# Optimization experiments

Hardware: AMD Instinct MI355X
Metric: run time of the kernel (lower is better)

The kernel has to match this reference:

```python
import jax, jax.numpy as jnp
import numpy as np
import math

B, S, E, H = 2, 2048, 1024, 16
D = E // H  # d_head = 64

def setup_inputs() -> dict:
    key = jax.random.key(0)
    ks = jax.random.split(key, 7)
    query = jax.random.normal(ks[0], (B, S, E), dtype=jnp.float32)
    k_in = jax.random.normal(ks[1], (B, S, E), dtype=jnp.float32)
    v_in = jax.random.normal(ks[2], (B, S, E), dtype=jnp.float32)
    # causal mask, broadcastable over batch and heads; mask==0 positions are blocked
    mask = jnp.tril(jnp.ones((S, S), dtype=jnp.int32))[None, None]
    scale = 1.0 / math.sqrt(E)
    w_q = jax.random.normal(ks[3], (E, E), dtype=jnp.float32) * scale
    w_k = jax.random.normal(ks[4], (E, E), dtype=jnp.float32) * scale
    w_v = jax.random.normal(ks[5], (E, E), dtype=jnp.float32) * scale
    w_o = jax.random.normal(ks[6], (E, E), dtype=jnp.float32) * scale
    return {"query": query, "key": k_in, "value": v_in, "mask": mask,
            "w_q": w_q, "w_k": w_k, "w_v": w_v, "w_o": w_o}

def reference(query, key, value, mask, w_q, w_k, w_v, w_o):
    # projections (nn.Linear with no bias: x @ W^T); split heads -> [B,H,S,D]
    q = (query @ w_q.T).reshape(B, S, H, D).transpose(0, 2, 1, 3)
    k = (key @ w_k.T).reshape(B, S, H, D).transpose(0, 2, 1, 3)
    v = (value @ w_v.T).reshape(B, S, H, D).transpose(0, 2, 1, 3)
    # scaled dot-product scores [B,H,S,S]
    scores = jnp.einsum('bhqd,bhkd->bhqk', q, k) / math.sqrt(D)
    scores = jnp.where(mask == 0, jnp.float32(-1e9), scores)
    attn = jax.nn.softmax(scores, axis=-1)  # dropout p=0.0 -> identity
    out = jnp.einsum('bhqk,bhkd->bhqd', attn, v)  # [B,H,S,D]
    out = out.transpose(0, 2, 1, 3).reshape(B, S, E)
    return out @ w_o.T
```

## Files before the change

kernel.cpp:

```cpp
#include <hip/hip_runtime.h>
#include <hip/hip_bf16.h>

#define B_ 2
#define S_ 2048
#define E_ 1024
#define H_ 16
#define D_ 64

typedef __attribute__((ext_vector_type(8))) short bf16x8;
typedef __attribute__((ext_vector_type(4))) float f32x4;

static __device__ __forceinline__ unsigned short f2bf(float x) {
    union { float f; unsigned u; } v; v.f = x;
    unsigned r = v.u + 0x7FFF + ((v.u >> 16) & 1);
    return (unsigned short)(r >> 16);
}

static __device__ __forceinline__ unsigned pack2bf(float a, float b) {
    union { float f; unsigned u; } x, y; x.f = a; y.f = b;
    unsigned ra = x.u + 0x7FFF + ((x.u >> 16) & 1);
    unsigned rb = y.u + 0x7FFF + ((y.u >> 16) & 1);
    return (ra >> 16) | (rb & 0xFFFF0000u);
}

static __device__ __forceinline__ unsigned packtrunc(float a, float b) {
    union { float f; unsigned u; } x, y; x.f = a; y.f = b;
    return __builtin_amdgcn_perm(y.u, x.u, 0x07060302);
}

static __device__ __forceinline__ void async_copy16(const void* gsrc, void* ldst) {
    __builtin_amdgcn_global_load_lds(
        (const __attribute__((address_space(1))) void*)gsrc,
        (__attribute__((address_space(3))) void*)ldst, 16, 0, 0);
}

__global__ void cvt_all(const float* __restrict__ s0, const float* __restrict__ s1,
                        const float* __restrict__ s2, const float* __restrict__ s3,
                        const float* __restrict__ s4, const float* __restrict__ s5,
                        const float* __restrict__ s6,
                        unsigned short* __restrict__ xdst, unsigned short* __restrict__ wdst,
                        float scq) {
    int b = blockIdx.x;
    const float* src; unsigned short* dst; int i; float c = 1.f;
    if (b < 12288) {
        int ti = b >> 12, lb = b & 4095;
        src = (ti == 0) ? s0 : (ti == 1) ? s1 : s2;
        dst = xdst + (size_t)ti * 4194304;
        i = lb * 256 + threadIdx.x;
    } else {
        int r = b - 12288, ti = r >> 10, lb = r & 1023;
        src = (ti == 0) ? s3 : (ti == 1) ? s4 : (ti == 2) ? s5 : s6;
        dst = wdst + (size_t)ti * 1048576;
        i = lb * 256 + threadIdx.x;
        if (ti == 0) c = scq;
    }
    float4 f = ((const float4*)src)[i];
    ushort4 o;
    o.x = f2bf(f.x * c); o.y = f2bf(f.y * c); o.z = f2bf(f.z * c); o.w = f2bf(f.w * c);
    ((ushort4*)dst)[i] = o;
}

__global__ __launch_bounds__(512, 2) void gemm256(
    const unsigned short* __restrict__ A0, const unsigned short* __restrict__ B0,
    void* __restrict__ C0) {
    __shared__ __align__(16) unsigned short L[65536];
    const int z = blockIdx.z;
    const unsigned short* A  = A0 + (size_t)z * 4194304;
    const unsigned short* Bm = B0 + (size_t)z * 1048576;
    const int o = (int)(blockIdx.x + (blockIdx.y << 2));
    const int cx = o & 7, tx = o >> 3;
    const int bm = (cx * 2 + (tx >> 2)) * 256;
    const int bn = (tx & 3) * 256;
    const int tid = threadIdx.x;
    const int w = tid >> 6, lane = tid & 63;
    const int wr = w >> 2, wc = w & 3;
    const int col = lane & 15, quad = lane >> 4;
    const int r0 = tid >> 3, cg = (tid & 7) ^ (r0 & 7);
    const size_t aR = (size_t)(bm + r0) * 1024 + cg * 8;
    const size_t bR = (size_t)(bn + r0) * 1024 + cg * 8;
    const int l0 = tid * 8, l1 = tid * 8 + 4096;
    const int ach = (quad ^ (col & 7)) * 8;
    const int aRd = wr * 8192 + col * 64 + ach;
    const int bRd = 32768 + (wc >> 1) * 8192 + (wc & 1) * 4096 + col * 64 + ach;

    f32x4 acc[8][4] = {};
    bf16x8 bA[4][2], bB0[2][2], bB1[2][2];

#define STAGE_A(d, h, t) do { \
    async_copy16(A + aR + (size_t)((h) * 128) * 1024 + (t) * 64, &L[((d) * 2 + (h)) * 8192 + l0]); \
    async_copy16(A + aR + (size_t)((h) * 128 + 64) * 1024 + (t) * 64, &L[((d) * 2 + (h)) * 8192 + l1]); \
} while (0)
#define STAGE_B(d, h, t) do { \
    async_copy16(Bm + bR + (size_t)((h) * 128) * 1024 + (t) * 64, &L[32768 + ((d) * 2 + (h)) * 8192 + l0]); \
    async_copy16(Bm + bR + (size_t)((h) * 128 + 64) * 1024 + (t) * 64, &L[32768 + ((d) * 2 + (h)) * 8192 + l1]); \
} while (0)
#define RD_A(d, mh) do { _Pragma("unroll") for (int i = 0; i < 4; i++) { \
    bA[i][0] = *(const bf16x8*)&L[(d) * 16384 + (mh) * 4096 + i * 1024 + aRd]; \
    bA[i][1] = *(const bf16x8*)&L[(d) * 16384 + (mh) * 4096 + i * 1024 + (aRd ^ 32)]; } } while (0)
#define RD_B(d, nh, BB) do { _Pragma("unroll") for (int j = 0; j < 2; j++) { \
    BB[j][0] = *(const bf16x8*)&L[(d) * 16384 + (nh) * 2048 + j * 1024 + bRd]; \
    BB[j][1] = *(const bf16x8*)&L[(d) * 16384 + (nh) * 2048 + j * 1024 + (bRd ^ 32)]; } } while (0)
#define MM(m0, BB, n0) do { __builtin_amdgcn_s_setprio(1); \
    _Pragma("unroll") for (int i = 0; i < 4; i++) _Pragma("unroll") for (int j = 0; j < 2; j++) { \
        acc[(m0) + i][(n0) + j] = __builtin_amdgcn_mfma_f32_16x16x32_bf16(bA[i][0], BB[j][0], acc[(m0) + i][(n0) + j], 0, 0, 0); \
        acc[(m0) + i][(n0) + j] = __builtin_amdgcn_mfma_f32_16x16x32_bf16(bA[i][1], BB[j][1], acc[(m0) + i][(n0) + j], 0, 0, 0); } \
    __builtin_amdgcn_s_setprio(0); } while (0)
#define BARX __builtin_amdgcn_s_barrier()
#define VMW asm volatile("s_waitcnt vmcnt(4)" ::: "memory")

    STAGE_B(0, 0, 0); STAGE_B(0, 1, 0);
    STAGE_A(0, 0, 0); STAGE_A(0, 1, 0);
    STAGE_B(1, 0, 1); STAGE_B(1, 1, 1);
    VMW; BARX;

#pragma unroll 1
    for (int j = 0; j < 8; j++) {
        const int to = 2 * j + 1;
        const int tn = (2 * j + 2 < 16) ? 2 * j + 2 : 15;
        const int tm = (2 * j + 3 < 16) ? 2 * j + 3 : 15;
        STAGE_A(1, 0, to); RD_A(0, 0); RD_B(0, 0, bB0); BARX; MM(0, bB0, 0); BARX;
        STAGE_A(1, 1, to); RD_B(0, 1, bB1);             BARX; MM(0, bB1, 2); BARX;
        STAGE_B(0, 0, tn); RD_A(0, 1);                  BARX; MM(4, bB1, 2); BARX;
        STAGE_B(0, 1, tn);                              BARX; MM(4, bB0, 0); VMW; BARX;
        STAGE_A(0, 0, tn); RD_A(1, 0); RD_B(1, 0, bB0); BARX; MM(0, bB0, 0); BARX;
        STAGE_A(0, 1, tn); RD_B(1, 1, bB1);             BARX; MM(0, bB1, 2); BARX;
        STAGE_B(1, 0, tm); RD_A(1, 1);                  BARX; MM(4, bB1, 2); BARX;
        STAGE_B(1, 1, tm);                              BARX; MM(4, bB0, 0); VMW; BARX;
    }
#undef STAGE_A
#undef STAGE_B
#undef RD_A
#undef RD_B
#undef MM
#undef BARX
#undef VMW

    __syncthreads();

    unsigned short* scr = &L[w * 8192];
    const int grow0 = bm + wr * 128;
    const int b  = grow0 >> 11;
    const int s0 = grow0 & 2047;
    const int hh = (bn + wc * 64) >> 6;
    unsigned short* outp = (unsigned short*)C0 + (size_t)z * 4194304;
    if (z == 2) {
#pragma unroll
        for (int mi = 0; mi < 8; mi++)
#pragma unroll
            for (int nj = 0; nj < 4; nj++) {
                int n = nj * 16 + col;
                int c = mi * 2 + (quad >> 1);
                uint2 pk;
                pk.x = pack2bf(acc[mi][nj][0], acc[mi][nj][1]);
                pk.y = pack2bf(acc[mi][nj][2], acc[mi][nj][3]);
                *(uint2*)&scr[n * 128 + ((c ^ (n & 7)) << 3) + ((quad & 1) << 2)] = pk;
            }
        asm volatile("s_waitcnt lgkmcnt(0)" ::: "memory");
#pragma unroll
        for (int it = 0; it < 16; it++) {
            int slot = it * 64 + lane, n = slot >> 4, c = slot & 15;
            uint4 v = *(uint4*)&scr[n * 128 + ((c ^ (n & 7)) << 3)];
            *(uint4*)&outp[(((size_t)b * H_ + hh) * D_ + n) * S_ + s0 + c * 8] = v;
        }
    } else {
#pragma unroll
        for (int mi = 0; mi < 8; mi++)
#pragma unroll
            for (int nj = 0; nj < 4; nj++)
#pragma unroll
                for (int r = 0; r < 4; r++) {
                    int m = mi * 16 + quad * 4 + r, n = nj * 16 + col;
                    scr[m * 64 + (((n >> 3) ^ (m & 7)) << 3) + (n & 7)] = f2bf(acc[mi][nj][r]);
                }
        asm volatile("s_waitcnt lgkmcnt(0)" ::: "memory");
#pragma unroll
        for (int it = 0; it < 16; it++) {
            int slot = it * 64 + lane, m = slot >> 3, c = slot & 7;
            uint4 v = *(uint4*)&scr[m * 64 + ((c ^ (m & 7)) << 3)];
            *(uint4*)&outp[(((size_t)b * H_ + hh) * S_ + s0 + m) * (size_t)D_ + c * 8] = v;
        }
    }
}

template <int MODE>
__global__ __launch_bounds__(256) void gemm128(
    const unsigned short* __restrict__ A0, const unsigned short* __restrict__ B0,
    void* __restrict__ C0, int M, int N, int K) {
    __shared__ __align__(16) unsigned short KV[8][4096];
    const unsigned short* A = A0;
    const unsigned short* Bm = B0;
    const int o = (int)(blockIdx.x + (blockIdx.y << 3));
    const int cx = o & 7, tx = o >> 3;
    const int bm = ((cx << 2) + (tx >> 3)) * 128;
    const int bn = (tx & 7) * 128;
    const int tid = threadIdx.x;
    const int w = tid >> 6, lane = tid & 63;
    const int col = lane & 15, quad = lane >> 4;
    const int wm = (w >> 1) * 64, wn = (w & 1) * 64;
    const int cq = (quad ^ ((col >> 1) & 3)) << 3;

    f32x4 acc[4][4] = {};

    const int r0 = tid >> 2;
    const int cg = (tid & 3) ^ ((r0 >> 1) & 3);
    const size_t aoff0 = (size_t)(bm + r0) * K + cg * 8;
    const size_t aoff1 = (size_t)(bm + r0 + 64) * K + cg * 8;
    const size_t boff0 = (size_t)(bn + r0) * K + cg * 8;
    const size_t boff1 = (size_t)(bn + r0 + 64) * K + cg * 8;
    const int l0 = tid * 8, l1 = (tid + 256) * 8;

    const int nk = K >> 5;

    async_copy16(A  + aoff0,      &KV[0][l0]);
    async_copy16(A  + aoff1,      &KV[0][l1]);
    async_copy16(Bm + boff0,      &KV[4][l0]);
    async_copy16(Bm + boff1,      &KV[4][l1]);
    async_copy16(A  + aoff0 + 32, &KV[1][l0]);
    async_copy16(A  + aoff1 + 32, &KV[1][l1]);
    async_copy16(Bm + boff0 + 32, &KV[5][l0]);
    async_copy16(Bm + boff1 + 32, &KV[5][l1]);

    for (int kt = 0; kt < nk; kt++) {
        {
            const int kp = kt + 2;
            const int src = (kp < nk) ? kp : (nk - 1);
            const int bp = kp & 3;
            const size_t ko = (size_t)src * 32;
            async_copy16(A  + aoff0 + ko, &KV[bp][l0]);
            async_copy16(A  + aoff1 + ko, &KV[bp][l1]);
            async_copy16(Bm + boff0 + ko, &KV[4 + bp][l0]);
            async_copy16(Bm + boff1 + ko, &KV[4 + bp][l1]);
        }
        asm volatile("s_waitcnt vmcnt(8)" ::: "memory");
        __builtin_amdgcn_s_barrier();

        const unsigned short* Ab = &KV[kt & 3][0];
        const unsigned short* Bb = &KV[4 + (kt & 3)][0];
        bf16x8 af[4], bfr[4];
#pragma unroll
        for (int i = 0; i < 4; i++) af[i]  = *(const bf16x8*)&Ab[(wm + i * 16 + col) * 32 + cq];
#pragma unroll
        for (int j = 0; j < 4; j++) bfr[j] = *(const bf16x8*)&Bb[(wn + j * 16 + col) * 32 + cq];
#pragma unroll
        for (int i = 0; i < 4; i++)
#pragma unroll
            for (int j = 0; j < 4; j++)
                acc[i][j] = __builtin_amdgcn_mfma_f32_16x16x32_bf16(af[i], bfr[j], acc[i][j], 0, 0, 0);
    }

    __syncthreads();

    if (MODE == 3) {
#pragma unroll
        for (int i = 0; i < 4; i++)
#pragma unroll
            for (int j = 0; j < 4; j++)
#pragma unroll
                for (int r = 0; r < 4; r++) {
                    int gm = bm + wm + i * 16 + quad * 4 + r;
                    int gn = bn + wn + j * 16 + col;
                    ((float*)C0)[(size_t)gm * N + gn] = acc[i][j][r];
                }
    }
}

__global__ __launch_bounds__(512) void attn_kernel(
    const unsigned short* __restrict__ Q, const unsigned short* __restrict__ K_,
    const unsigned short* __restrict__ Vt, unsigned short* __restrict__ Out) {
    __shared__ __align__(16) unsigned short KV[8][4096];
    __shared__ __align__(16) float Lred[4][2][64];
    const int o = (int)(blockIdx.x + (blockIdx.y << 4));
    const int cx = o & 7, tx = o >> 3;
    const int hloc = (tx >> 1) & 3;
    const int f_ = (tx ^ (tx >> 5)) & 1;
    const int G_ = (((tx >> 4) & 1) << 2) | (((tx >> 3) & 1) << 1) | (tx & 1);
    const int qb = f_ ? (G_ ^ 15) : G_;
    const int bh = (cx << 2) + hloc;
    const int q0 = qb * 128;
    const int tid = threadIdx.x;
    const int w = tid >> 6, lane = tid & 63;
    const int qg = w >> 1, kh = w & 1, kh32 = kh << 5;
    const int col = lane & 15, quad = lane >> 4, swz = col & 7;
    const int qw0 = q0 + qg * 32;
    const float NINF = -__builtin_huge_valf();

    const unsigned short* Qh = Q + (size_t)bh * S_ * D_;
    const unsigned short* Kh = K_ + (size_t)bh * S_ * D_;
    const unsigned short* Vh = Vt + (size_t)bh * D_ * S_;

    bf16x8 qf[2][2];
#pragma unroll
    for (int i = 0; i < 2; i++)
#pragma unroll
        for (int h = 0; h < 2; h++)
            qf[i][h] = *(const bf16x8*)(Qh + (size_t)(qw0 + i * 16 + col) * 64 + h * 32 + quad * 8);

    f32x4 o_[2][4] = {};
    float lsum[2] = {0.f, 0.f};

    const int sRow = tid >> 3, sCg = (tid & 7) ^ (sRow & 7);
    const size_t koff = (size_t)sRow * 64 + sCg * 8;
    const size_t voff = (size_t)sRow * S_ + sCg * 8;
    const int ldsoff = tid * 8;

    const int nk = 2 * (qb + 1);

    async_copy16(Kh + koff, &KV[0][ldsoff]);
    async_copy16(Vh + voff, &KV[4][ldsoff]);
    async_copy16(Kh + koff + 64 * 64, &KV[1][ldsoff]);
    async_copy16(Vh + voff + 64, &KV[5][ldsoff]);

    for (int kt = 0; kt < nk; kt++) {
        const int k0 = kt * 64;
        {
            const int kp = kt + 2;
            const int src = (kp < nk) ? kp : (nk - 1);
            const int bp = kp & 3;
            async_copy16(Kh + koff + (size_t)src * 4096, &KV[bp][ldsoff]);
            async_copy16(Vh + voff + (size_t)src * 64, &KV[4 + bp][ldsoff]);
        }
        asm volatile("s_waitcnt vmcnt(4)" ::: "memory");
        __builtin_amdgcn_s_barrier();

        if (k0 + kh32 > qw0 + 31) continue;

        const unsigned short* Kb = &KV[kt & 3][0];
        const unsigned short* Vb = &KV[4 + (kt & 3)][0];

        f32x4 sc[2][2] = {};
        __builtin_amdgcn_s_setprio(1);
#pragma unroll
        for (int h = 0; h < 2; h++) {
            const int cq = ((h * 4 + quad) ^ swz) * 8;
#pragma unroll
            for (int ct = 0; ct < 2; ct++) {
                bf16x8 kf = *(const bf16x8*)&Kb[(kh32 + ct * 16 + col) * 64 + cq];
                sc[0][ct] = __builtin_amdgcn_mfma_f32_16x16x32_bf16(kf, qf[0][h], sc[0][ct], 0, 0, 0);
                sc[1][ct] = __builtin_amdgcn_mfma_f32_16x16x32_bf16(kf, qf[1][h], sc[1][ct], 0, 0, 0);
            }
        }
        __builtin_amdgcn_s_setprio(0);
        if (k0 + kh32 + 31 <= qw0) {
#pragma unroll
            for (int i = 0; i < 2; i++)
#pragma unroll
                for (int ct = 0; ct < 2; ct++) {
#pragma unroll
                    for (int r = 0; r < 4; r++)
                        sc[i][ct][r] = __builtin_amdgcn_exp2f(sc[i][ct][r]);
                    lsum[i] += (sc[i][ct][0] + sc[i][ct][1]) + (sc[i][ct][2] + sc[i][ct][3]);
                }
        } else {
#pragma unroll
            for (int i = 0; i < 2; i++)
#pragma unroll
                for (int ct = 0; ct < 2; ct++) {
#pragma unroll
                    for (int r = 0; r < 4; r++) {
                        int key = k0 + kh32 + ct * 16 + quad * 4 + r;
                        int qidx = qw0 + i * 16 + col;
                        float s = (key <= qidx) ? sc[i][ct][r] : NINF;
                        sc[i][ct][r] = __builtin_amdgcn_exp2f(s);
                    }
                    lsum[i] += (sc[i][ct][0] + sc[i][ct][1]) + (sc[i][ct][2] + sc[i][ct][3]);
                }
        }
        union { bf16x8 v; unsigned u[4]; } pf[2];
#pragma unroll
        for (int i = 0; i < 2; i++) {
            pf[i].u[0] = packtrunc(sc[i][0][0], sc[i][0][1]);
            pf[i].u[1] = packtrunc(sc[i][0][2], sc[i][0][3]);
            pf[i].u[2] = packtrunc(sc[i][1][0], sc[i][1][1]);
            pf[i].u[3] = packtrunc(sc[i][1][2], sc[i][1][3]);
        }
        __builtin_amdgcn_s_setprio(1);
#pragma unroll
        for (int dt = 0; dt < 4; dt++) {
            const int row = dt * 16 + col;
            const int ko0 = kh32 + quad * 4;
            const int ko1 = ko0 + 16;
            union { bf16x8 v; uint2 d2[2]; } vf;
            vf.d2[0] = *(const uint2*)&Vb[row * 64 + (((ko0 >> 3) ^ (row & 7)) << 3) + (ko0 & 7)];
            vf.d2[1] = *(const uint2*)&Vb[row * 64 + (((ko1 >> 3) ^ (row & 7)) << 3) + (ko1 & 7)];
#pragma unroll
            for (int i = 0; i < 2; i++)
                o_[i][dt] = __builtin_amdgcn_mfma_f32_16x16x32_bf16(vf.v, pf[i].v, o_[i][dt], 0, 0, 0);
        }
        __builtin_amdgcn_s_setprio(0);
    }

    __syncthreads();
    if (kh == 1) {
        f32x4* R = (f32x4*)&KV[0][0] + qg * 512 + lane * 8;
#pragma unroll
        for (int i = 0; i < 2; i++)
#pragma unroll
            for (int dt = 0; dt < 4; dt++) R[i * 4 + dt] = o_[i][dt];
        Lred[qg][0][lane] = lsum[0];
        Lred[qg][1][lane] = lsum[1];
    }
    __syncthreads();
    if (kh == 0) {
        f32x4* R = (f32x4*)&KV[0][0] + qg * 512 + lane * 8;
#pragma unroll
        for (int i = 0; i < 2; i++)
#pragma unroll
            for (int dt = 0; dt < 4; dt++) o_[i][dt] += R[i * 4 + dt];
        lsum[0] += Lred[qg][0][lane];
        lsum[1] += Lred[qg][1][lane];

        const int b = bh >> 4, hh = bh & 15;
#pragma unroll
        for (int i = 0; i < 2; i++) {
            float l = lsum[i];
            l += __shfl_xor(l, 16);
            l += __shfl_xor(l, 32);
            float inv = 1.f / l;
            int gq = qw0 + i * 16 + col;
#pragma unroll
            for (int dt = 0; dt < 4; dt++) {
                uint2 pk;
                pk.x = pack2bf(o_[i][dt][0] * inv, o_[i][dt][1] * inv);
                pk.y = pack2bf(o_[i][dt][2] * inv, o_[i][dt][3] * inv);
                *(uint2*)&Out[((size_t)b * S_ + gq) * E_ + hh * 64 + dt * 16 + quad * 4] = pk;
            }
        }
    }
}

extern "C" void kernel_launch(void* const* d_in, const int* in_sizes, int n_in,
                              void* d_out, int out_size, void* d_ws, size_t ws_size,
                              hipStream_t stream) {
    const float* query = (const float*)d_in[0];
    const float* key_i = (const float*)d_in[1];
    const float* value = (const float*)d_in[2];
    const float* w_q = (const float*)d_in[4];
    const float* w_k = (const float*)d_in[5];
    const float* w_v = (const float*)d_in[6];
    const float* w_o = (const float*)d_in[7];
    float* out = (float*)d_out;

    const int M = B_ * S_;
    const int N = E_, K = E_;

    char* ws = (char*)d_ws;
    unsigned short* xq  = (unsigned short*)(ws);
    unsigned short* wqb = (unsigned short*)(ws + (24u << 20));
    unsigned short* Qb  = (unsigned short*)(ws + (32u << 20));
    unsigned short* Kb  = (unsigned short*)(ws + (40u << 20));
    unsigned short* Vtb = (unsigned short*)(ws + (48u << 20));
    unsigned short* Ab  = (unsigned short*)(ws + (56u << 20));

    const float SCQ = 0.125f * 1.44269504088896f;

    cvt_all<<<16384, 256, 0, stream>>>(query, key_i, value, w_q, w_k, w_v, w_o,
                                       xq, wqb, SCQ);

    gemm256<<<dim3(4, 16, 3), 512, 0, stream>>>(xq, wqb, Qb);

    attn_kernel<<<dim3(S_ / 128, B_ * H_), 512, 0, stream>>>(Qb, Kb, Vtb, Ab);

    gemm128<3><<<dim3(8, 32), 256, 0, stream>>>(
        Ab, wqb + 3u * 1048576u, out, M, N, K);
}
```

Measured before the change: 204.6 us.

## Software-pipeline attention loop: overlap QK^T of tile t with softmax/PV of t-1

Restructures the attention inner loop so each iteration computes the QK^T scores for the current key tile while running exp, pack and PV MFMAs for the previous tile, using two ping-pong score register sets and a manually unrolled-by-two loop. V tiles are now prefetched one step ahead instead of two, and V is stored so one 16-byte LDS read replaces two 8-byte reads. It also sets a waves-per-EU hint in launch_bounds and changes the transposed V store in the projection epilogue to permute key positions to match the new V fragment layout. The aim is to hide MFMA and exp latency behind each other, at the cost of higher register pressure and a more fragile buffer-reuse schedule.

Result: no change. 202.5 us (-1.0%).

```diff
diff --git a/kernel.cpp b/kernel.cpp
--- a/kernel.cpp
+++ b/kernel.cpp
@@ -157,10 +157,14 @@
             }
         asm volatile("s_waitcnt lgkmcnt(0)" ::: "memory");
 #pragma unroll
-        for (int it = 0; it < 16; it++) {
-            int slot = it * 64 + lane, n = slot >> 4, c = slot & 15;
-            uint4 v = *(uint4*)&scr[n * 128 + ((c ^ (n & 7)) << 3)];
-            *(uint4*)&outp[(((size_t)b * H_ + hh) * D_ + n) * S_ + s0 + c * 8] = v;
+        for (int it = 0; it < 32; it++) {
+            int slot = it * 64 + lane;
+            int n = slot >> 5, u = slot & 31;
+            int grp = u >> 3, T = u & 7;
+            int kpos = grp * 32 + (T & 1) * 16 + ((T >> 1) & 3) * 4;
+            int c = kpos >> 3, off = kpos & 7;
+            uint2 v = *(uint2*)&scr[n * 128 + ((c ^ (n & 7)) << 3) + off];
+            *(uint2*)&outp[(((size_t)b * H_ + hh) * D_ + n) * S_ + s0 + grp * 32 + T * 4] = v;
         }
     } else {
 #pragma unroll
@@ -264,7 +268,7 @@
     }
 }
 
-__global__ __launch_bounds__(512) void attn_kernel(
+__global__ __launch_bounds__(512, 4) void attn_kernel(
     const unsigned short* __restrict__ Q, const unsigned short* __restrict__ K_,
     const unsigned short* __restrict__ Vt, unsigned short* __restrict__ Out) {
     __shared__ __align__(16) unsigned short KV[8][4096];
@@ -297,97 +301,90 @@
 
     f32x4 o_[2][4] = {};
     float lsum[2] = {0.f, 0.f};
+    f32x4 scA[2][2], scB[2][2];
 
     const int sRow = tid >> 3, sCg = (tid & 7) ^ (sRow & 7);
     const size_t koff = (size_t)sRow * 64 + sCg * 8;
     const size_t voff = (size_t)sRow * S_ + sCg * 8;
     const int ldsoff = tid * 8;
+    const int vch = ((kh * 4 + quad) ^ (col & 7)) << 3;
 
     const int nk = 2 * (qb + 1);
 
     async_copy16(Kh + koff, &KV[0][ldsoff]);
+    async_copy16(Kh + koff + 4096, &KV[1][ldsoff]);
     async_copy16(Vh + voff, &KV[4][ldsoff]);
-    async_copy16(Kh + koff + 64 * 64, &KV[1][ldsoff]);
-    async_copy16(Vh + voff + 64, &KV[5][ldsoff]);
-
-    for (int kt = 0; kt < nk; kt++) {
-        const int k0 = kt * 64;
-        {
-            const int kp = kt + 2;
-            const int src = (kp < nk) ? kp : (nk - 1);
-            const int bp = kp & 3;
-            async_copy16(Kh + koff + (size_t)src * 4096, &KV[bp][ldsoff]);
-            async_copy16(Vh + voff + (size_t)src * 64, &KV[4 + bp][ldsoff]);
-        }
-        asm volatile("s_waitcnt vmcnt(4)" ::: "memory");
-        __builtin_amdgcn_s_barrier();
-
-        if (k0 + kh32 > qw0 + 31) continue;
-
-        const unsigned short* Kb = &KV[kt & 3][0];
-        const unsigned short* Vb = &KV[4 + (kt & 3)][0];
-
-        f32x4 sc[2][2] = {};
-        __builtin_amdgcn_s_setprio(1);
-#pragma unroll
-        for (int h = 0; h < 2; h++) {
-            const int cq = ((h * 4 + quad) ^ swz) * 8;
-#pragma unroll
-            for (int ct = 0; ct < 2; ct++) {
-                bf16x8 kf = *(const bf16x8*)&Kb[(kh32 + ct * 16 + col) * 64 + cq];
-                sc[0][ct] = __builtin_amdgcn_mfma_f32_16x16x32_bf16(kf, qf[0][h], sc[0][ct], 0, 0, 0);
-                sc[1][ct] = __builtin_amdgcn_mfma_f32_16x16x32_bf16(kf, qf[1][h], sc[1][ct], 0, 0, 0);
-            }
-        }
-        __builtin_amdgcn_s_setprio(0);
-        if (k0 + kh32 + 31 <= qw0) {
-#pragma unroll
-            for (int i = 0; i < 2; i++)
-#pragma unroll
-                for (int ct = 0; ct < 2; ct++) {
-#pragma unroll
-                    for (int r = 0; r < 4; r++)
-                        sc[i][ct][r] = __builtin_amdgcn_exp2f(sc[i][ct][r]);
-                    lsum[i] += (sc[i][ct][0] + sc[i][ct][1]) + (sc[i][ct][2] + sc[i][ct][3]);
-                }
-        } else {
-#pragma unroll
-            for (int i = 0; i < 2; i++)
-#pragma unroll
-                for (int ct = 0; ct < 2; ct++) {
-#pragma unroll
-                    for (int r = 0; r < 4; r++) {
-                        int key = k0 + kh32 + ct * 16 + quad * 4 + r;
-                        int qidx = qw0 + i * 16 + col;
-                        float s = (key <= qidx) ? sc[i][ct][r] : NINF;
-                        sc[i][ct][r] = __builtin_amdgcn_exp2f(s);
-                    }
-                    lsum[i] += (sc[i][ct][0] + sc[i][ct][1]) + (sc[i][ct][2] + sc[i][ct][3]);
-                }
-        }
-        union { bf16x8 v; unsigned u[4]; } pf[2];
-#pragma unroll
-        for (int i = 0; i < 2; i++) {
-            pf[i].u[0] = packtrunc(sc[i][0][0], sc[i][0][1]);
-            pf[i].u[1] = packtrunc(sc[i][0][2], sc[i][0][3]);
-            pf[i].u[2] = packtrunc(sc[i][1][0], sc[i][1][1]);
-            pf[i].u[3] = packtrunc(sc[i][1][2], sc[i][1][3]);
-        }
-        __builtin_amdgcn_s_setprio(1);
-#pragma unroll
-        for (int dt = 0; dt < 4; dt++) {
-            const int row = dt * 16 + col;
-            const int ko0 = kh32 + quad * 4;
-            const int ko1 = ko0 + 16;
-            union { bf16x8 v; uint2 d2[2]; } vf;
-            vf.d2[0] = *(const uint2*)&Vb[row * 64 + (((ko0 >> 3) ^ (row & 7)) << 3) + (ko0 & 7)];
-            vf.d2[1] = *(const uint2*)&Vb[row * 64 + (((ko1 >> 3) ^ (row & 7)) << 3) + (ko1 & 7)];
-#pragma unroll
-            for (int i = 0; i < 2; i++)
-                o_[i][dt] = __builtin_amdgcn_mfma_f32_16x16x32_bf16(vf.v, pf[i].v, o_[i][dt], 0, 0, 0);
-        }
-        __builtin_amdgcn_s_setprio(0);
-    }
+
+#define APROC(T, PRV) do { \
+    const int k0p = (T) * 64; \
+    if (k0p + kh32 + 31 <= qw0) { \
+        _Pragma("unroll") for (int i2 = 0; i2 < 2; i2++) \
+        _Pragma("unroll") for (int c2 = 0; c2 < 2; c2++) { \
+            _Pragma("unroll") for (int r2 = 0; r2 < 4; r2++) \
+                PRV[i2][c2][r2] = __builtin_amdgcn_exp2f(PRV[i2][c2][r2]); \
+            lsum[i2] += (PRV[i2][c2][0] + PRV[i2][c2][1]) + (PRV[i2][c2][2] + PRV[i2][c2][3]); } \
+    } else { \
+        _Pragma("unroll") for (int i2 = 0; i2 < 2; i2++) \
+        _Pragma("unroll") for (int c2 = 0; c2 < 2; c2++) { \
+            _Pragma("unroll") for (int r2 = 0; r2 < 4; r2++) { \
+                int key = k0p + kh32 + c2 * 16 + quad * 4 + r2; \
+                int qidx = qw0 + i2 * 16 + col; \
+                float sv = (key <= qidx) ? PRV[i2][c2][r2] : NINF; \
+                PRV[i2][c2][r2] = __builtin_amdgcn_exp2f(sv); } \
+            lsum[i2] += (PRV[i2][c2][0] + PRV[i2][c2][1]) + (PRV[i2][c2][2] + PRV[i2][c2][3]); } \
+    } \
+    union { bf16x8 v; unsigned u[4]; } pf[2]; \
+    _Pragma("unroll") for (int i2 = 0; i2 < 2; i2++) { \
+        pf[i2].u[0] = packtrunc(PRV[i2][0][0], PRV[i2][0][1]); \
+        pf[i2].u[1] = packtrunc(PRV[i2][0][2], PRV[i2][0][3]); \
+        pf[i2].u[2] = packtrunc(PRV[i2][1][0], PRV[i2][1][1]); \
+        pf[i2].u[3] = packtrunc(PRV[i2][1][2], PRV[i2][1][3]); } \
+    const unsigned short* Vbp = &KV[4 + ((T) & 3)][0]; \
+    __builtin_amdgcn_s_setprio(1); \
+    _Pragma("unroll") for (int dt = 0; dt < 4; dt++) { \
+        bf16x8 vf = *(const bf16x8*)&Vbp[(dt * 16 + col) * 64 + vch]; \
+        _Pragma("unroll") for (int i2 = 0; i2 < 2; i2++) \
+            o_[i2][dt] = __builtin_amdgcn_mfma_f32_16x16x32_bf16(vf, pf[i2].v, o_[i2][dt], 0, 0, 0); } \
+    __builtin_amdgcn_s_setprio(0); \
+} while (0)
+
+#define AITER(KT, CUR, PRV, DOPRV) do { \
+    const int kti = (KT); \
+    { const int kp = kti + 2; const int srcK = (kp < nk) ? kp : (nk - 1); \
+      async_copy16(Kh + koff + (size_t)srcK * 4096, &KV[kp & 3][ldsoff]); \
+      const int vp = kti + 1; const int srcV = (vp < nk) ? vp : (nk - 1); \
+      async_copy16(Vh + voff + (size_t)srcV * 64, &KV[4 + (vp & 3)][ldsoff]); } \
+    asm volatile("s_waitcnt vmcnt(4)" ::: "memory"); \
+    __builtin_amdgcn_s_barrier(); \
+    if (kti * 64 + kh32 <= qw0 + 31) { \
+        const unsigned short* Kb = &KV[kti & 3][0]; \
+        _Pragma("unroll") for (int i2 = 0; i2 < 2; i2++) \
+        _Pragma("unroll") for (int c2 = 0; c2 < 2; c2++) \
+        _Pragma("unroll") for (int r2 = 0; r2 < 4; r2++) CUR[i2][c2][r2] = 0.f; \
+        __builtin_amdgcn_s_setprio(1); \
+        _Pragma("unroll") for (int h = 0; h < 2; h++) { \
+            const int cqh = ((h * 4 + quad) ^ swz) * 8; \
+            _Pragma("unroll") for (int ct = 0; ct < 2; ct++) { \
+                bf16x8 kf = *(const bf16x8*)&Kb[(kh32 + ct * 16 + col) * 64 + cqh]; \
+                CUR[0][ct] = __builtin_amdgcn_mfma_f32_16x16x32_bf16(kf, qf[0][h], CUR[0][ct], 0, 0, 0); \
+                CUR[1][ct] = __builtin_amdgcn_mfma_f32_16x16x32_bf16(kf, qf[1][h], CUR[1][ct], 0, 0, 0); } } \
+        __builtin_amdgcn_s_setprio(0); \
+    } \
+    if ((DOPRV) && (kti - 1) * 64 + kh32 <= qw0 + 31) APROC(kti - 1, PRV); \
+} while (0)
+
+    AITER(0, scA, scB, 0);
+    AITER(1, scB, scA, 1);
+#pragma unroll 1
+    for (int kt = 2; kt < nk; kt += 2) {
+        AITER(kt, scA, scB, 1);
+        AITER(kt + 1, scB, scA, 1);
+    }
+    asm volatile("s_waitcnt vmcnt(0)" ::: "memory");
+    __builtin_amdgcn_s_barrier();
+    if ((nk - 1) * 64 + kh32 <= qw0 + 31) APROC(nk - 1, scB);
+#undef AITER
+#undef APROC
 
     __syncthreads();
     if (kh == 1) {
```
